# Optimization experiments

Measured on AMD Instinct MI355X. Metric: run time of the kernel, lower is better.

The kernel has to match this reference:

```python
import jax, jax.numpy as jnp
import numpy as np

MASKED = True


def setup_inputs() -> dict:
    key = jax.random.key(0)
    kq, kk, kv = jax.random.split(key, 3)
    shape = (4, 16, 2048, 64)  # [B, H, S, d]
    q = jax.random.normal(kq, shape, dtype=jnp.float32)
    k = jax.random.normal(kk, shape, dtype=jnp.float32)
    v = jax.random.normal(kv, shape, dtype=jnp.float32)
    return {"q": q, "k": k, "v": v}


def reference(q, k, v):
    d = k.shape[-1]
    scale = 1.0 / jnp.sqrt(jnp.asarray(d, dtype=q.dtype))
    # [B, H, S, S]
    att = jnp.einsum("bhqd,bhkd->bhqk", q, k) * scale
    if MASKED:
        # Faithful to torch source: tril of the scores, then mask where zero
        tri = jnp.tril(att)
        att = jnp.where(tri == 0, -jnp.inf, att)
    att = jax.nn.softmax(att, axis=-1)
    return jnp.einsum("bhqk,bhkd->bhqd", att, v)
```

## Files before the change

### kernel.cpp

```cpp
#include <hip/hip_runtime.h>
#include <hip/hip_bf16.h>

typedef __attribute__((ext_vector_type(8)))  short bf16x8;
typedef __attribute__((ext_vector_type(4)))  float f32x4;
typedef __attribute__((ext_vector_type(16))) float f32x16;
typedef unsigned short ushort_t;

#define S_LEN 2048
#define D_DIM 64
#define FIXED_M 14.0f

#if __has_builtin(__builtin_amdgcn_exp2f)
#define EXP2(x) __builtin_amdgcn_exp2f(x)
#else
#define EXP2(x) __expf((x) * 0.6931471805599453f)
#endif

__device__ __forceinline__ short f2bf(float f) {
  union { float f; unsigned u; } x; x.f = f;
  unsigned r = x.u + 0x7fffu + ((x.u >> 16) & 1u);
  return (short)(r >> 16);
}

__device__ __forceinline__ unsigned cvtpk_bf16(float lo, float hi) {
  unsigned r;
  asm("v_cvt_pk_bf16_f32 %0, %1, %2" : "=v"(r) : "v"(lo), "v"(hi));
  return r;
}

__device__ __forceinline__ void pl32swap(unsigned& a, unsigned& b) {
  asm volatile("v_permlane32_swap_b32 %0, %1" : "+v"(a), "+v"(b));
}

__device__ __forceinline__ void gl_lds16(const ushort_t* g, ushort_t* l) {
  __builtin_amdgcn_global_load_lds(
      (const __attribute__((address_space(1))) unsigned*)g,
      (__attribute__((address_space(3))) unsigned*)l, 16, 0, 0);
}

__global__ void prep_kernel(const float* __restrict__ Kf, const float* __restrict__ Vf,
                            ushort_t* __restrict__ Kb, ushort_t* __restrict__ Vt) {
  if (blockIdx.x < 2048) {
    const long n8 = (long)64 * S_LEN * D_DIM / 8;
    long i = (long)blockIdx.x * blockDim.x + threadIdx.x;
    const long stride = (long)2048 * blockDim.x;
    for (; i < n8; i += stride) {
      const float4* p = (const float4*)(Kf + i * 8);
      float4 a = p[0], b = p[1];
      bf16x8 t;
      t[0]=f2bf(a.x); t[1]=f2bf(a.y); t[2]=f2bf(a.z); t[3]=f2bf(a.w);
      t[4]=f2bf(b.x); t[5]=f2bf(b.y); t[6]=f2bf(b.z); t[7]=f2bf(b.w);
      *(bf16x8*)(Kb + i * 8) = t;
    }
  } else {
    const int bid = blockIdx.x - 2048;
    const int h  = bid >> 5;
    const int s0 = (bid & 31) * 64;
    const float* Vh = Vf + (size_t)h * S_LEN * D_DIM;
    ushort_t* Vth   = Vt + (size_t)h * D_DIM * S_LEN;
    __shared__ float tile[64][65];
    const int r  = threadIdx.x >> 2;
    const int c4 = (threadIdx.x & 3) * 16;
#pragma unroll
    for (int j = 0; j < 16; j += 4) {
      float4 x = *(const float4*)(Vh + (size_t)(s0 + r) * D_DIM + c4 + j);
      tile[r][c4 + j + 0] = x.x; tile[r][c4 + j + 1] = x.y;
      tile[r][c4 + j + 2] = x.z; tile[r][c4 + j + 3] = x.w;
    }
    __syncthreads();
    bf16x8 o0, o1;
#pragma unroll
    for (int j = 0; j < 8; ++j) o0[j] = f2bf(tile[c4 + j][r]);
#pragma unroll
    for (int j = 0; j < 8; ++j) o1[j] = f2bf(tile[c4 + 8 + j][r]);
    *(bf16x8*)(Vth + (size_t)r * S_LEN + s0 + c4)     = o0;
    *(bf16x8*)(Vth + (size_t)r * S_LEN + s0 + c4 + 8) = o1;
  }
}

__global__ __launch_bounds__(256, 2)
void flash32_kernel(const float* __restrict__ Qf, const ushort_t* __restrict__ Kb,
                    const ushort_t* __restrict__ Vt, float* __restrict__ Og) {
  const int tid = threadIdx.x;
  const int l   = tid & 63;
  const int wv  = tid >> 6;
  const int hi  = l >> 5;
  const int l31 = l & 31;
  const int l7  = l & 7;
  const int l8  = l >> 3;

  const int bid  = blockIdx.x;
  const int r6   = bid & 63;
  const int head = (r6 & 7) * 8 + (r6 >> 3);
  const int p    = bid >> 6;
  const int qhiQ = 15 - p;
  const int qloQ = p;

  const float*    Qh = Qf + (size_t)head * S_LEN * D_DIM;
  const ushort_t* Kh = Kb + (size_t)head * S_LEN * D_DIM;
  const ushort_t* Vh = Vt + (size_t)head * D_DIM * S_LEN;
  float*          Oh = Og + (size_t)head * S_LEN * D_DIM;

  __shared__ ushort_t smK[2][64 * 64];
  __shared__ ushort_t smV[2][64 * 64];

  const int swsrc = (l7 ^ l8) * 8;
  const int rb    = l31 * 64;

#define STAGE_K(T, B) do {                                                 \
    const int kvk_ = (T) * 64;                                             \
    _Pragma("unroll")                                                      \
    for (int u_ = 0; u_ < 2; ++u_) {                                       \
      const int idx_ = wv * 2 + u_;                                        \
      const int row_ = idx_ * 8 + l8;                                      \
      gl_lds16(Kh + (size_t)(kvk_ + row_) * 64 + swsrc,                    \
               &smK[B][idx_ * 512]);                                       \
    }                                                                      \
  } while (0)

#define STAGE_V(T, B) do {                                                 \
    const int kvv_ = (T) * 64;                                             \
    _Pragma("unroll")                                                      \
    for (int u_ = 0; u_ < 2; ++u_) {                                       \
      const int idx_ = wv * 2 + u_;                                        \
      const int d_ = idx_ * 8 + l8;                                        \
      gl_lds16(Vh + (size_t)d_ * S_LEN + kvv_ + swsrc,                     \
               &smV[B][idx_ * 512]);                                       \
    }                                                                      \
  } while (0)

#define VMCNT0() asm volatile("s_waitcnt vmcnt(0)" ::: "memory")
#define BAR()    __builtin_amdgcn_s_barrier()

#define QKT(S0, S1, KB) do {                                               \
    _Pragma("unroll")                                                      \
    for (int i = 0; i < 16; ++i) { S0[i] = -FIXED_M; S1[i] = -FIXED_M; }   \
    const ushort_t* kb_ = smK[KB];                                         \
    __builtin_amdgcn_s_setprio(1);                                         \
    _Pragma("unroll")                                                      \
    for (int ks = 0; ks < 4; ++ks) {                                       \
      const int ch = ((ks * 2 + hi) ^ l7) * 8;                             \
      bf16x8 a0 = *(const bf16x8*)(kb_ + rb + ch);                         \
      bf16x8 a1 = *(const bf16x8*)(kb_ + 2048 + rb + ch);                  \
      S0 = __builtin_amdgcn_mfma_f32_32x32x16_bf16(a0, qf[ks], S0, 0, 0, 0); \
      S1 = __builtin_amdgcn_mfma_f32_32x32x16_bf16(a1, qf[ks], S1, 0, 0, 0); \
    }                                                                      \
    __builtin_amdgcn_s_setprio(0);                                         \
  } while (0)

#define SOFTMAX(S0, S1, KV0) do {                                          \
    if ((KV0) + 63 > qminw) {                                              \
      _Pragma("unroll")                                                    \
      for (int r = 0; r < 16; ++r) {                                       \
        const int crow = (r & 3) + 8 * (r >> 2) + 4 * hi;                  \
        if ((KV0) + crow > qrow)      S0[r] = -INFINITY;                   \
        if ((KV0) + 32 + crow > qrow) S1[r] = -INFINITY;                   \
      }                                                                    \
    }                                                                      \
    _Pragma("unroll")                                                      \
    for (int i = 0; i < 16; ++i) S0[i] = EXP2(S0[i]);                      \
    _Pragma("unroll")                                                      \
    for (int i = 0; i < 16; ++i) S1[i] = EXP2(S1[i]);                      \
    float b8[8];                                                           \
    _Pragma("unroll")                                                      \
    for (int i = 0; i < 8; ++i)                                            \
      b8[i] = (S0[i] + S0[i+8]) + (S1[i] + S1[i+8]);                       \
    _Pragma("unroll")                                                      \
    for (int i = 0; i < 4; ++i) b8[i] += b8[i+4];                          \
    l_run += (b8[0] + b8[2]) + (b8[1] + b8[3]);                            \
    _Pragma("unroll")                                                      \
    for (int ks = 0; ks < 4; ++ks) {                                       \
      const int r0 = (ks & 1) * 8;                                         \
      unsigned w0, w1, w2, w3;                                             \
      if (ks < 2) {                                                        \
        w0 = cvtpk_bf16(S0[r0+0], S0[r0+1]); w2 = cvtpk_bf16(S0[r0+4], S0[r0+5]); \
        w1 = cvtpk_bf16(S0[r0+2], S0[r0+3]); w3 = cvtpk_bf16(S0[r0+6], S0[r0+7]); \
      } else {                                                             \
        w0 = cvtpk_bf16(S1[r0+0], S1[r0+1]); w2 = cvtpk_bf16(S1[r0+4], S1[r0+5]); \
        w1 = cvtpk_bf16(S1[r0+2], S1[r0+3]); w3 = cvtpk_bf16(S1[r0+6], S1[r0+7]); \
      }                                                                    \
      pl32swap(w0, w2); pl32swap(w1, w3);                                  \
      union { unsigned u[4]; bf16x8 v; } pu_;                              \
      pu_.u[0] = w0; pu_.u[1] = w1; pu_.u[2] = w2; pu_.u[3] = w3;          \
      pw[ks] = pu_.v;                                                      \
    }                                                                      \
  } while (0)

#define PV(VB) do {                                                        \
    const ushort_t* vb_ = smV[VB];                                         \
    __builtin_amdgcn_s_setprio(1);                                         \
    _Pragma("unroll")                                                      \
    for (int ks = 0; ks < 4; ++ks) {                                       \
      const int ch = ((ks * 2 + hi) ^ l7) * 8;                             \
      bf16x8 va  = *(const bf16x8*)(vb_ + rb + ch);                        \
      bf16x8 vB2 = *(const bf16x8*)(vb_ + 2048 + rb + ch);                 \
      accA = __builtin_amdgcn_mfma_f32_32x32x16_bf16(va,  pw[ks], accA, 0, 0, 0); \
      accB = __builtin_amdgcn_mfma_f32_32x32x16_bf16(vB2, pw[ks], accB, 0, 0, 0); \
    }                                                                      \
    __builtin_amdgcn_s_setprio(0);                                         \
  } while (0)

  for (int seg = 0; seg < 2; ++seg) {
    const int qidx = seg ? qloQ : qhiQ;
    const int q0   = qidx * 128;
    const int nt   = 2 * qidx + 2;

    const int qrow  = q0 + wv * 32 + l31;
    const int qminw = q0 + wv * 32;

    if (seg) BAR();

    STAGE_K(0, 0);
    STAGE_V(0, 0);
    STAGE_K(1, 1);

    bf16x8 qf[4];
    {
      const float sc = 0.125f * 1.44269504089f;
      const float* qp = Qh + (size_t)qrow * D_DIM + 8 * hi;
#pragma unroll
      for (int ks = 0; ks < 4; ++ks) {
        float4 x = *(const float4*)(qp + ks * 16);
        float4 y = *(const float4*)(qp + ks * 16 + 4);
        bf16x8 t;
        t[0]=f2bf(x.x*sc); t[1]=f2bf(x.y*sc);
        t[2]=f2bf(x.z*sc); t[3]=f2bf(x.w*sc);
        t[4]=f2bf(y.x*sc); t[5]=f2bf(y.y*sc);
        t[6]=f2bf(y.z*sc); t[7]=f2bf(y.w*sc);
        qf[ks] = t;
      }
    }

    f32x16 accA, accB, sA0, sA1, sB0, sB1;
#pragma unroll
    for (int i = 0; i < 16; ++i) { accA[i] = 0.f; accB[i] = 0.f; }
    float l_run = 0.f;
    bf16x8 pw[4];

    VMCNT0();
    BAR();
    QKT(sA0, sA1, 0);

    for (int t = 0; t + 2 < nt; t += 2) {
      VMCNT0(); BAR();
      STAGE_K(t + 2, 0);
      STAGE_V(t + 1, 1);
      QKT(sB0, sB1, 1);
      SOFTMAX(sA0, sA1, t * 64);
      PV(0);
      VMCNT0(); BAR();
      STAGE_K(t + 3, 1);
      STAGE_V(t + 2, 0);
      QKT(sA0, sA1, 0);
      SOFTMAX(sB0, sB1, (t + 1) * 64);
      PV(1);
    }
    {
      const int t = nt - 2;
      VMCNT0(); BAR();
      STAGE_V(t + 1, 1);
      QKT(sB0, sB1, 1);
      SOFTMAX(sA0, sA1, t * 64);
      PV(0);
      VMCNT0(); BAR();
      SOFTMAX(sB0, sB1, (t + 1) * 64);
      PV(1);
    }

    l_run += __shfl_xor(l_run, 32, 64);
    const float inv = 1.0f / l_run;
    float* op = Oh + (size_t)qrow * D_DIM + 4 * hi;
#pragma unroll
    for (int m4 = 0; m4 < 4; ++m4) {
      float4 a = { accA[4*m4+0]*inv, accA[4*m4+1]*inv,
                   accA[4*m4+2]*inv, accA[4*m4+3]*inv };
      *(float4*)(op + 8 * m4) = a;
      float4 b = { accB[4*m4+0]*inv, accB[4*m4+1]*inv,
                   accB[4*m4+2]*inv, accB[4*m4+3]*inv };
      *(float4*)(op + 32 + 8 * m4) = b;
    }
  }

#undef STAGE_K
#undef STAGE_V
#undef VMCNT0
#undef BAR
#undef QKT
#undef SOFTMAX
#undef PV
}

#define BQ 64
#define BK 64
#define LDK 72
#define LDP 72

__device__ __forceinline__ unsigned pack_bf(float lo, float hi) {
  return (unsigned)(unsigned short)f2bf(lo) |
         ((unsigned)(unsigned short)f2bf(hi) << 16);
}

__global__ __launch_bounds__(256, 2)
void flash_fwd_kernel(const float* __restrict__ Qg, const float* __restrict__ Kg,
                      const float* __restrict__ Vg, float* __restrict__ Og) {
  const int tid  = threadIdx.x;
  const int lane = tid & 63;
  const int wv   = tid >> 6;
  const int grp  = lane >> 4;
  const int l16  = lane & 15;
  const int bid = blockIdx.x;
  const int qb  = 31 - (bid & 31);
  const int bh  = bid >> 5;
  const int q0  = qb * BQ;
  const size_t hoff = (size_t)bh * S_LEN * D_DIM;
  const float* Qh = Qg + hoff;
  const float* Kh = Kg + hoff;
  const float* Vh = Vg + hoff;
  float*       Oh = Og + hoff;
  __shared__ short sK [BK][LDK];
  __shared__ short sVT[D_DIM][LDP];
  __shared__ short sP [4][16][LDP];
  bf16x8 qf[2];
  {
    const float* qrow = Qh + (size_t)(q0 + wv*16 + l16) * D_DIM + grp*8;
#pragma unroll
    for (int kc = 0; kc < 2; ++kc) {
      float4 a = *reinterpret_cast<const float4*>(qrow + kc*32);
      float4 b = *reinterpret_cast<const float4*>(qrow + kc*32 + 4);
      bf16x8 t;
      t[0]=f2bf(a.x*0.125f); t[1]=f2bf(a.y*0.125f);
      t[2]=f2bf(a.z*0.125f); t[3]=f2bf(a.w*0.125f);
      t[4]=f2bf(b.x*0.125f); t[5]=f2bf(b.y*0.125f);
      t[6]=f2bf(b.z*0.125f); t[7]=f2bf(b.w*0.125f);
      qf[kc] = t;
    }
  }
  f32x4 acc[4];
#pragma unroll
  for (int nb = 0; nb < 4; ++nb) acc[nb] = (f32x4){0.f, 0.f, 0.f, 0.f};
  float m_i[4] = {-INFINITY, -INFINITY, -INFINITY, -INFINITY};
  float l_i[4] = {0.f, 0.f, 0.f, 0.f};
  const int srow = tid >> 2;
  const int scb  = tid & 3;
  for (int kt = 0; kt <= qb; ++kt) {
    const int kv0 = kt * BK;
    __syncthreads();
    {
      const float* src = Kh + (size_t)(kv0 + srow) * D_DIM + scb*16;
      float4 x0 = *reinterpret_cast<const float4*>(src);
      float4 x1 = *reinterpret_cast<const float4*>(src + 4);
      float4 x2 = *reinterpret_cast<const float4*>(src + 8);
      float4 x3 = *reinterpret_cast<const float4*>(src + 12);
      bf16x8 lo, hi;
      lo[0]=f2bf(x0.x); lo[1]=f2bf(x0.y); lo[2]=f2bf(x0.z); lo[3]=f2bf(x0.w);
      lo[4]=f2bf(x1.x); lo[5]=f2bf(x1.y); lo[6]=f2bf(x1.z); lo[7]=f2bf(x1.w);
      hi[0]=f2bf(x2.x); hi[1]=f2bf(x2.y); hi[2]=f2bf(x2.z); hi[3]=f2bf(x2.w);
      hi[4]=f2bf(x3.x); hi[5]=f2bf(x3.y); hi[6]=f2bf(x3.z); hi[7]=f2bf(x3.w);
      *reinterpret_cast<bf16x8*>(&sK[srow][scb*16])     = lo;
      *reinterpret_cast<bf16x8*>(&sK[srow][scb*16 + 8]) = hi;
    }
    {
      const float* src = Vh + (size_t)(kv0 + scb*16) * D_DIM + srow;
      bf16x8 lo, hi;
#pragma unroll
      for (int j = 0; j < 8; ++j) lo[j] = f2bf(src[(size_t)j * D_DIM]);
#pragma unroll
      for (int j = 0; j < 8; ++j) hi[j] = f2bf(src[(size_t)(j + 8) * D_DIM]);
      *reinterpret_cast<bf16x8*>(&sVT[srow][scb*16])     = lo;
      *reinterpret_cast<bf16x8*>(&sVT[srow][scb*16 + 8]) = hi;
    }
    __syncthreads();
    f32x4 sc[4];
#pragma unroll
    for (int nb = 0; nb < 4; ++nb) {
      f32x4 c = (f32x4){0.f, 0.f, 0.f, 0.f};
#pragma unroll
      for (int kc = 0; kc < 2; ++kc) {
        bf16x8 kf = *reinterpret_cast<const bf16x8*>(&sK[nb*16 + l16][kc*32 + grp*8]);
        c = __builtin_amdgcn_mfma_f32_16x16x32_bf16(qf[kc], kf, c, 0, 0, 0);
      }
      sc[nb] = c;
    }
    const bool diag = (kt == qb);
#pragma unroll
    for (int r = 0; r < 4; ++r) {
      const int qi = wv*16 + grp*4 + r;
      float s0 = sc[0][r], s1 = sc[1][r], s2 = sc[2][r], s3 = sc[3][r];
      if (diag) {
        if (l16 +  0 > qi) s0 = -INFINITY;
        if (l16 + 16 > qi) s1 = -INFINITY;
        if (l16 + 32 > qi) s2 = -INFINITY;
        if (l16 + 48 > qi) s3 = -INFINITY;
      }
      float mx = fmaxf(fmaxf(s0, s1), fmaxf(s2, s3));
#pragma unroll
      for (int off = 8; off; off >>= 1)
        mx = fmaxf(mx, __shfl_xor(mx, off, 64));
      const float mn    = fmaxf(m_i[r], mx);
      const float alpha = __expf(m_i[r] - mn);
      const float p0 = __expf(s0 - mn);
      const float p1 = __expf(s1 - mn);
      const float p2 = __expf(s2 - mn);
      const float p3 = __expf(s3 - mn);
      float rs = (p0 + p1) + (p2 + p3);
#pragma unroll
      for (int off = 8; off; off >>= 1)
        rs += __shfl_xor(rs, off, 64);
      l_i[r] = l_i[r] * alpha + rs;
      m_i[r] = mn;
      acc[0][r] *= alpha; acc[1][r] *= alpha;
      acc[2][r] *= alpha; acc[3][r] *= alpha;
      const float n0 = __shfl_xor(p0, 1, 64);
      const float n1 = __shfl_xor(p1, 1, 64);
      const float n2 = __shfl_xor(p2, 1, 64);
      const float n3 = __shfl_xor(p3, 1, 64);
      if (!(lane & 1)) {
        const int prow = grp*4 + r;
        unsigned* base = reinterpret_cast<unsigned*>(&sP[wv][prow][l16]);
        base[0]  = pack_bf(p0, n0);
        base[8]  = pack_bf(p1, n1);
        base[16] = pack_bf(p2, n2);
        base[24] = pack_bf(p3, n3);
      }
    }
    bf16x8 pf[2];
#pragma unroll
    for (int kc = 0; kc < 2; ++kc)
      pf[kc] = *reinterpret_cast<const bf16x8*>(&sP[wv][l16][kc*32 + grp*8]);
#pragma unroll
    for (int nb = 0; nb < 4; ++nb) {
#pragma unroll
      for (int kc = 0; kc < 2; ++kc) {
        bf16x8 vf = *reinterpret_cast<const bf16x8*>(&sVT[l16 + 16*nb][kc*32 + grp*8]);
        acc[nb] = __builtin_amdgcn_mfma_f32_16x16x32_bf16(pf[kc], vf, acc[nb], 0, 0, 0);
      }
    }
  }
#pragma unroll
  for (int r = 0; r < 4; ++r) {
    const float inv = 1.0f / l_i[r];
    float* orow = Oh + (size_t)(q0 + wv*16 + grp*4 + r) * D_DIM + l16;
#pragma unroll
    for (int nb = 0; nb < 4; ++nb)
      orow[nb*16] = acc[nb][r] * inv;
  }
}

extern "C" void kernel_launch(void* const* d_in, const int* in_sizes, int n_in,
                              void* d_out, int out_size, void* d_ws, size_t ws_size,
                              hipStream_t stream) {
  (void)n_in; (void)out_size;
  const float* q = (const float*)d_in[0];
  const float* k = (const float*)d_in[1];
  const float* v = (const float*)d_in[2];
  float* o = (float*)d_out;
  const int bh = in_sizes[0] / (S_LEN * D_DIM);
  const size_t elems = (size_t)bh * S_LEN * D_DIM;

  if (ws_size >= elems * 2 * 2 && bh == 64) {
    ushort_t* Kb = (ushort_t*)d_ws;
    ushort_t* Vt = Kb + elems;
    prep_kernel<<<4096, 256, 0, stream>>>(k, v, Kb, Vt);
    flash32_kernel<<<bh * 8, 256, 0, stream>>>(q, Kb, Vt, o);
  } else {
    flash_fwd_kernel<<<bh * (S_LEN / BQ), 256, 0, stream>>>(q, k, v, o);
  }
}
```

Measured before the change: 70.45 us.

## Split KV tiles across wave pairs with 64-row Q blocks and LDS reduction

Each block now handles 64 query rows per segment instead of 128, and the grid doubles. The two waves of each pair process alternating KV tiles for the same 32 query rows, and their partial accumulators and row sums are merged through LDS at the end. The kernel uses four K/V LDS buffers, staging two tiles ahead, and synchronises once per pair of tiles. The aim is more parallelism and shorter per-wave dependency chains. The cost is double the LDS, an extra reduction and barriers, and the loss of the software pipelining that overlapped QK^T with softmax.

```diff
diff --git a/kernel.cpp b/kernel.cpp
--- a/kernel.cpp
+++ b/kernel.cpp
@@ -84,6 +84,8 @@
   const int tid = threadIdx.x;
   const int l   = tid & 63;
   const int wv  = tid >> 6;
+  const int g   = wv >> 1;
+  const int par = wv & 1;
   const int hi  = l >> 5;
   const int l31 = l & 31;
   const int l7  = l & 7;
@@ -93,78 +95,78 @@
   const int r6   = bid & 63;
   const int head = (r6 & 7) * 8 + (r6 >> 3);
   const int p    = bid >> 6;
-  const int qhiQ = 15 - p;
-  const int qloQ = p;
+  const int segA = 31 - p;
+  const int segB = p;
 
   const float*    Qh = Qf + (size_t)head * S_LEN * D_DIM;
   const ushort_t* Kh = Kb + (size_t)head * S_LEN * D_DIM;
   const ushort_t* Vh = Vt + (size_t)head * D_DIM * S_LEN;
   float*          Oh = Og + (size_t)head * S_LEN * D_DIM;
 
-  __shared__ ushort_t smK[2][64 * 64];
-  __shared__ ushort_t smV[2][64 * 64];
+  __shared__ ushort_t smK[4][64 * 64];
+  __shared__ ushort_t smV[4][64 * 64];
 
   const int swsrc = (l7 ^ l8) * 8;
   const int rb    = l31 * 64;
 
-#define STAGE_K(T, B) do {                                                 \
+#define STAGE_K(T) do {                                                    \
     const int kvk_ = (T) * 64;                                             \
+    ushort_t* dk_ = smK[(T) & 3];                                          \
     _Pragma("unroll")                                                      \
     for (int u_ = 0; u_ < 2; ++u_) {                                       \
       const int idx_ = wv * 2 + u_;                                        \
       const int row_ = idx_ * 8 + l8;                                      \
-      gl_lds16(Kh + (size_t)(kvk_ + row_) * 64 + swsrc,                    \
-               &smK[B][idx_ * 512]);                                       \
+      gl_lds16(Kh + (size_t)(kvk_ + row_) * 64 + swsrc, dk_ + idx_ * 512); \
     }                                                                      \
   } while (0)
 
-#define STAGE_V(T, B) do {                                                 \
+#define STAGE_V(T) do {                                                    \
     const int kvv_ = (T) * 64;                                             \
+    ushort_t* dv_ = smV[(T) & 3];                                          \
     _Pragma("unroll")                                                      \
     for (int u_ = 0; u_ < 2; ++u_) {                                       \
       const int idx_ = wv * 2 + u_;                                        \
       const int d_ = idx_ * 8 + l8;                                        \
-      gl_lds16(Vh + (size_t)d_ * S_LEN + kvv_ + swsrc,                     \
-               &smV[B][idx_ * 512]);                                       \
+      gl_lds16(Vh + (size_t)d_ * S_LEN + kvv_ + swsrc, dv_ + idx_ * 512);  \
     }                                                                      \
   } while (0)
 
 #define VMCNT0() asm volatile("s_waitcnt vmcnt(0)" ::: "memory")
 #define BAR()    __builtin_amdgcn_s_barrier()
 
-#define QKT(S0, S1, KB) do {                                               \
-    _Pragma("unroll")                                                      \
-    for (int i = 0; i < 16; ++i) { S0[i] = -FIXED_M; S1[i] = -FIXED_M; }   \
-    const ushort_t* kb_ = smK[KB];                                         \
+#define QKT(T) do {                                                        \
+    _Pragma("unroll")                                                      \
+    for (int i = 0; i < 16; ++i) { sS0[i] = -FIXED_M; sS1[i] = -FIXED_M; } \
+    const ushort_t* kb_ = smK[(T) & 3];                                    \
     __builtin_amdgcn_s_setprio(1);                                         \
     _Pragma("unroll")                                                      \
     for (int ks = 0; ks < 4; ++ks) {                                       \
       const int ch = ((ks * 2 + hi) ^ l7) * 8;                             \
       bf16x8 a0 = *(const bf16x8*)(kb_ + rb + ch);                         \
       bf16x8 a1 = *(const bf16x8*)(kb_ + 2048 + rb + ch);                  \
-      S0 = __builtin_amdgcn_mfma_f32_32x32x16_bf16(a0, qf[ks], S0, 0, 0, 0); \
-      S1 = __builtin_amdgcn_mfma_f32_32x32x16_bf16(a1, qf[ks], S1, 0, 0, 0); \
+      sS0 = __builtin_amdgcn_mfma_f32_32x32x16_bf16(a0, qf[ks], sS0, 0, 0, 0); \
+      sS1 = __builtin_amdgcn_mfma_f32_32x32x16_bf16(a1, qf[ks], sS1, 0, 0, 0); \
     }                                                                      \
     __builtin_amdgcn_s_setprio(0);                                         \
   } while (0)
 
-#define SOFTMAX(S0, S1, KV0) do {                                          \
+#define SOFTMAX(KV0) do {                                                  \
     if ((KV0) + 63 > qminw) {                                              \
       _Pragma("unroll")                                                    \
       for (int r = 0; r < 16; ++r) {                                       \
         const int crow = (r & 3) + 8 * (r >> 2) + 4 * hi;                  \
-        if ((KV0) + crow > qrow)      S0[r] = -INFINITY;                   \
-        if ((KV0) + 32 + crow > qrow) S1[r] = -INFINITY;                   \
+        if ((KV0) + crow > qrow)      sS0[r] = -INFINITY;                  \
+        if ((KV0) + 32 + crow > qrow) sS1[r] = -INFINITY;                  \
       }                                                                    \
     }                                                                      \
     _Pragma("unroll")                                                      \
-    for (int i = 0; i < 16; ++i) S0[i] = EXP2(S0[i]);                      \
-    _Pragma("unroll")                                                      \
-    for (int i = 0; i < 16; ++i) S1[i] = EXP2(S1[i]);                      \
+    for (int i = 0; i < 16; ++i) sS0[i] = EXP2(sS0[i]);                    \
+    _Pragma("unroll")                                                      \
+    for (int i = 0; i < 16; ++i) sS1[i] = EXP2(sS1[i]);                    \
     float b8[8];                                                           \
     _Pragma("unroll")                                                      \
     for (int i = 0; i < 8; ++i)                                            \
-      b8[i] = (S0[i] + S0[i+8]) + (S1[i] + S1[i+8]);                       \
+      b8[i] = (sS0[i] + sS0[i+8]) + (sS1[i] + sS1[i+8]);                   \
     _Pragma("unroll")                                                      \
     for (int i = 0; i < 4; ++i) b8[i] += b8[i+4];                          \
     l_run += (b8[0] + b8[2]) + (b8[1] + b8[3]);                            \
@@ -173,11 +175,11 @@
       const int r0 = (ks & 1) * 8;                                         \
       unsigned w0, w1, w2, w3;                                             \
       if (ks < 2) {                                                        \
-        w0 = cvtpk_bf16(S0[r0+0], S0[r0+1]); w2 = cvtpk_bf16(S0[r0+4], S0[r0+5]); \
-        w1 = cvtpk_bf16(S0[r0+2], S0[r0+3]); w3 = cvtpk_bf16(S0[r0+6], S0[r0+7]); \
+        w0 = cvtpk_bf16(sS0[r0+0], sS0[r0+1]); w2 = cvtpk_bf16(sS0[r0+4], sS0[r0+5]); \
+        w1 = cvtpk_bf16(sS0[r0+2], sS0[r0+3]); w3 = cvtpk_bf16(sS0[r0+6], sS0[r0+7]); \
       } else {                                                             \
-        w0 = cvtpk_bf16(S1[r0+0], S1[r0+1]); w2 = cvtpk_bf16(S1[r0+4], S1[r0+5]); \
-        w1 = cvtpk_bf16(S1[r0+2], S1[r0+3]); w3 = cvtpk_bf16(S1[r0+6], S1[r0+7]); \
+        w0 = cvtpk_bf16(sS1[r0+0], sS1[r0+1]); w2 = cvtpk_bf16(sS1[r0+4], sS1[r0+5]); \
+        w1 = cvtpk_bf16(sS1[r0+2], sS1[r0+3]); w3 = cvtpk_bf16(sS1[r0+6], sS1[r0+7]); \
       }                                                                    \
       pl32swap(w0, w2); pl32swap(w1, w3);                                  \
       union { unsigned u[4]; bf16x8 v; } pu_;                              \
@@ -186,8 +188,8 @@
     }                                                                      \
   } while (0)
 
-#define PV(VB) do {                                                        \
-    const ushort_t* vb_ = smV[VB];                                         \
+#define PV(T) do {                                                         \
+    const ushort_t* vb_ = smV[(T) & 3];                                    \
     __builtin_amdgcn_s_setprio(1);                                         \
     _Pragma("unroll")                                                      \
     for (int ks = 0; ks < 4; ++ks) {                                       \
@@ -201,18 +203,16 @@
   } while (0)
 
   for (int seg = 0; seg < 2; ++seg) {
-    const int qidx = seg ? qloQ : qhiQ;
-    const int q0   = qidx * 128;
-    const int nt   = 2 * qidx + 2;
-
-    const int qrow  = q0 + wv * 32 + l31;
-    const int qminw = q0 + wv * 32;
-
-    if (seg) BAR();
-
-    STAGE_K(0, 0);
-    STAGE_V(0, 0);
-    STAGE_K(1, 1);
+    const int sq   = seg ? segB : segA;
+    const int q0   = sq * 64;
+    const int nt   = sq + 1;
+
+    const int qrow  = q0 + g * 32 + l31;
+    const int qminw = q0 + g * 32;
+
+    STAGE_K(0);
+    STAGE_V(0);
+    if (nt > 1) { STAGE_K(1); STAGE_V(1); }
 
     bf16x8 qf[4];
     {
@@ -231,7 +231,7 @@
       }
     }
 
-    f32x16 accA, accB, sA0, sA1, sB0, sB1;
+    f32x16 accA, accB, sS0, sS1;
 #pragma unroll
     for (int i = 0; i < 16; ++i) { accA[i] = 0.f; accB[i] = 0.f; }
     float l_run = 0.f;
@@ -239,45 +239,53 @@
 
     VMCNT0();
     BAR();
-    QKT(sA0, sA1, 0);
-
-    for (int t = 0; t + 2 < nt; t += 2) {
-      VMCNT0(); BAR();
-      STAGE_K(t + 2, 0);
-      STAGE_V(t + 1, 1);
-      QKT(sB0, sB1, 1);
-      SOFTMAX(sA0, sA1, t * 64);
-      PV(0);
-      VMCNT0(); BAR();
-      STAGE_K(t + 3, 1);
-      STAGE_V(t + 2, 0);
-      QKT(sA0, sA1, 0);
-      SOFTMAX(sB0, sB1, (t + 1) * 64);
-      PV(1);
-    }
+
+    for (int t = 0; t < nt; t += 2) {
+      if (t + 2 < nt) { STAGE_K(t + 2); STAGE_V(t + 2); }
+      if (t + 3 < nt) { STAGE_K(t + 3); STAGE_V(t + 3); }
+      const int myt = t + par;
+      if (myt < nt) {
+        QKT(myt);
+        SOFTMAX(myt * 64);
+        PV(myt);
+      }
+      VMCNT0();
+      BAR();
+    }
+
     {
-      const int t = nt - 2;
-      VMCNT0(); BAR();
-      STAGE_V(t + 1, 1);
-      QKT(sB0, sB1, 1);
-      SOFTMAX(sA0, sA1, t * 64);
-      PV(0);
-      VMCNT0(); BAR();
-      SOFTMAX(sB0, sB1, (t + 1) * 64);
-      PV(1);
-    }
-
-    l_run += __shfl_xor(l_run, 32, 64);
-    const float inv = 1.0f / l_run;
-    float* op = Oh + (size_t)qrow * D_DIM + 4 * hi;
-#pragma unroll
-    for (int m4 = 0; m4 < 4; ++m4) {
-      float4 a = { accA[4*m4+0]*inv, accA[4*m4+1]*inv,
-                   accA[4*m4+2]*inv, accA[4*m4+3]*inv };
-      *(float4*)(op + 8 * m4) = a;
-      float4 b = { accB[4*m4+0]*inv, accB[4*m4+1]*inv,
-                   accB[4*m4+2]*inv, accB[4*m4+3]*inv };
-      *(float4*)(op + 32 + 8 * m4) = b;
+      float* cb = (float*)&smK[0][0] + g * 2176;
+      if (par == 0) {
+#pragma unroll
+        for (int i = 0; i < 16; ++i) {
+          cb[i * 64 + l]        = accA[i];
+          cb[(16 + i) * 64 + l] = accB[i];
+        }
+        l_run += __shfl_xor(l_run, 32, 64);
+        cb[2048 + l31] = l_run;
+      }
+      BAR();
+      if (par == 1) {
+#pragma unroll
+        for (int i = 0; i < 16; ++i) {
+          accA[i] += cb[i * 64 + l];
+          accB[i] += cb[(16 + i) * 64 + l];
+        }
+        l_run += __shfl_xor(l_run, 32, 64);
+        l_run += cb[2048 + l31];
+        const float inv = 1.0f / l_run;
+        float* op = Oh + (size_t)qrow * D_DIM + 4 * hi;
+#pragma unroll
+        for (int m4 = 0; m4 < 4; ++m4) {
+          float4 a = { accA[4*m4+0]*inv, accA[4*m4+1]*inv,
+                       accA[4*m4+2]*inv, accA[4*m4+3]*inv };
+          *(float4*)(op + 8 * m4) = a;
+          float4 b = { accB[4*m4+0]*inv, accB[4*m4+1]*inv,
+                       accB[4*m4+2]*inv, accB[4*m4+3]*inv };
+          *(float4*)(op + 32 + 8 * m4) = b;
+        }
+      }
+      BAR();
     }
   }
 
@@ -461,7 +469,7 @@
     ushort_t* Kb = (ushort_t*)d_ws;
     ushort_t* Vt = Kb + elems;
     prep_kernel<<<4096, 256, 0, stream>>>(k, v, Kb, Vt);
-    flash32_kernel<<<bh * 8, 256, 0, stream>>>(q, Kb, Vt, o);
+    flash32_kernel<<<bh * 16, 256, 0, stream>>>(q, Kb, Vt, o);
   } else {
     flash_fwd_kernel<<<bh * (S_LEN / BQ), 256, 0, stream>>>(q, k, v, o);
   }
```

Measured after the change: 83.92 us. 19.1% more time.
